# Optimization experiments

Hardware: AMD Instinct MI355X
Metric: run time of the kernel (lower is better)

## Reference

```python
import jax, jax.numpy as jnp
import numpy as np

# Detect.__init__ defaults from the source
TOP_K = 5000
CONF_THRESH = 0.01
NMS_THRESH = 0.3
VAR0, VAR1 = 0.1, 0.2   # variance = [0.1, 0.2]
NUM_CLASSES = 2

B = 16
IMAGE = 1280
FMAPS = [320, 160, 80, 40, 20, 10]          # image / steps [4,8,16,32,64,128]
MIN_SIZES = [16, 32, 64, 128, 256, 512]
AR = 1.5                                     # aspect_ratios = [[1.5]] * 6


def make_priors():
    """Vectorized PriorBox.forward: 1 prior per location (max_sizes=[], single AR)."""
    chunks = []
    for f, ms in zip(FMAPS, MIN_SIZES):
        c = (np.arange(f, dtype=np.float32) + 0.5) / f
        cy, cx = np.meshgrid(c, c, indexing='ij')
        s = ms / float(IMAGE)
        w = np.full_like(cx, s / np.sqrt(AR))   # s_k / sqrt(ar)
        h = np.full_like(cx, s * np.sqrt(AR))   # s_k * sqrt(ar)
        chunks.append(np.stack([cx, cy, w, h], -1).reshape(-1, 4))
    pr = np.concatenate(chunks, 0).clip(0.0, 1.0)   # clip=True
    return jnp.asarray(pr, jnp.float32)             # [136500, 4]


def setup_inputs() -> dict:
    key = jax.random.key(0)
    k1, k2 = jax.random.split(key)
    P = sum(f * f for f in FMAPS)   # 136500
    loc_data = 0.5 * jax.random.normal(k1, (B, P, 4), jnp.float32)
    conf_data = jax.random.uniform(k2, (B * P, NUM_CLASSES), jnp.float32)  # post-softmax probs
    prior_data = make_priors()
    return {"loc_data": loc_data, "conf_data": conf_data, "prior_data": prior_data}


def _decode(loc, priors):
    # SSD box decode with variances [0.1, 0.2]; loc, priors: [P,4]
    cxcy = priors[:, :2] + loc[:, :2] * VAR0 * priors[:, 2:]
    wh = priors[:, 2:] * jnp.exp(loc[:, 2:] * VAR1)
    xy1 = cxcy - wh * 0.5
    xy2 = xy1 + wh
    return jnp.concatenate([xy1, xy2], axis=-1)   # [P,4] x1y1x2y2


def _greedy_keep(boxes, valid):
    # Greedy NMS over score-sorted candidates. boxes [K,4], valid [K] bool.
    # Indices/keep decisions are discrete -> computed on stop_gradient'd boxes.
    b = jax.lax.stop_gradient(boxes)
    x1, y1, x2, y2 = b[:, 0], b[:, 1], b[:, 2], b[:, 3]
    area = (x2 - x1) * (y2 - y1)
    idxs = jnp.arange(b.shape[0])

    def body(keep, i):
        iw = jnp.maximum(jnp.minimum(x2, x2[i]) - jnp.maximum(x1, x1[i]), 0.0)
        ih = jnp.maximum(jnp.minimum(y2, y2[i]) - jnp.maximum(y1, y1[i]), 0.0)
        inter = iw * ih
        iou = inter / (area + area[i] - inter)
        suppress = keep[i] & (iou > NMS_THRESH) & (idxs > i)
        return keep & ~suppress, None

    keep, _ = jax.lax.scan(body, valid, idxs)
    return keep


def _detect_one(loc_i, conf_cl, priors):
    # loc_i [P,4]; conf_cl [P] = class-1 scores; returns [TOP_K, 5] (score, x1,y1,x2,y2)
    boxes = _decode(loc_i, priors)
    masked = jnp.where(conf_cl > CONF_THRESH, conf_cl, -1.0)   # c_mask gating
    order = jnp.argsort(-jax.lax.stop_gradient(masked))[:TOP_K]  # scores.sort, top_k cap
    s = masked[order]
    b = boxes[order]
    valid = s > CONF_THRESH
    keep = _greedy_keep(b, valid)
    # scatter kept (score, box) rows, in descending-score order, into dense output
    rank = jnp.cumsum(keep) - 1
    row = jnp.where(keep, rank, TOP_K)            # dropped rows -> scratch slot
    vals = jnp.concatenate([s[:, None], b], axis=1)
    vals = jnp.where(keep[:, None], vals, 0.0)
    out = jnp.zeros((TOP_K + 1, 5), jnp.float32).at[row].set(vals)
    return out[:TOP_K]


def reference(loc_data, conf_data, prior_data):
    num = loc_data.shape[0]
    P = prior_data.shape[0]
    conf_preds = conf_data.reshape(num, P, NUM_CLASSES).transpose(0, 2, 1)  # [B,2,P]
    cls1 = jax.vmap(_detect_one, in_axes=(0, 0, None))(loc_data, conf_preds[:, 1, :], prior_data)
    bg = jnp.zeros_like(cls1)                     # background class row stays zero
    output = jnp.stack([bg, cls1], axis=1)        # [B, 2, TOP_K, 5]
    # NOTE: the original's final `flt[(rank < top_k)...].fill_(0)` fills a boolean-indexed
    # COPY in torch, so it is a no-op on `output`; we faithfully return output unchanged.
    return output
```

## Files before the change

kernel.cpp:

```cpp
#include <hip/hip_runtime.h>
#include <math.h>

#pragma clang fp contract(off)

#define PNUM 136500
#define HPNUM 68250
#define BNUM 16
#define TOPK 5000
#define CAP 8192
#define NB4 4096
#define WBASE 0x2F000u
#define GCS 4
#define NWORDS 79
#define NW32 158
#define GSTRIDE 32
#define CAPE 65536
#define ELDS 10240
#define NXB 128
#define NWC 8
#define NXB2 1024
#define BSTRIDE 5120
#define EBUF 3072
#define SLOTS 4
#define SKI(i) ((i) + ((i) >> 4))

#define OFF_SC    ((size_t)0)
#define OFF_BOX4  (OFF_SC + 320000)
#define OFF_HIST  (OFF_BOX4 + 1280000)
#define OFF_GBCUR (OFF_HIST + 262144)
#define OFF_ECNT  (OFF_GBCUR + 1048576)
#define OFF_BCNT  (OFF_ECNT + 2048)
#define OFF_BCUR  (OFF_BCNT + 65536)
#define OFF_WCNT  (OFF_BCUR + 65536)
#define OFF_ZEND  (OFF_WCNT + 64)
#define OFF_CUT   (OFF_ZEND)
#define OFF_SBASE (OFF_CUT + 64)
#define OFF_WL    (OFF_SBASE + 262144)
#define OFF_KEYS  (OFF_WL + 262144)
#define OFF_EDGE  (OFF_KEYS + 1048576)
#define OFF_GRP   (OFF_EDGE + 4194304)
#define OFF_BOFS  (OFF_GRP)
#define OFF_SIDX  (OFF_GRP + 16384)
#define OFF_SBOX  (OFF_SIDX + 327680)

__device__ __forceinline__ unsigned f2ord(float f) {
    unsigned u = __float_as_uint(f);
    return (u & 0x80000000u) ? ~u : (u | 0x80000000u);
}
__device__ __forceinline__ float ord2f(unsigned o) {
    unsigned u = (o & 0x80000000u) ? (o ^ 0x80000000u) : ~o;
    return __uint_as_float(u);
}
__device__ __forceinline__ int bucketOf(float x) {
    int b = (int)((x + 0.6f) * 71.111115f);
    return (b < 0) ? 0 : ((b > 127) ? 127 : b);
}
__device__ __forceinline__ int rkeyOf(float x1, float x2) {
    int b = bucketOf(x1);
    int wc = bucketOf(x2) - b;
    if (wc > NWC - 1) wc = NWC - 1;
    if (wc < 0) wc = 0;
    return b * NWC + wc;
}

__global__ void __launch_bounds__(512) k_hist(const float* __restrict__ conf,
                                              unsigned* __restrict__ hist) {
    __shared__ unsigned lh[NB4];
    int img = blockIdx.y;
    for (int i = threadIdx.x; i < NB4; i += 512) lh[i] = 0;
    __syncthreads();
    const float4* src = (const float4*)(conf + (size_t)img * PNUM * 2);
    int stride = gridDim.x * 512;
    for (int q = blockIdx.x * 512 + threadIdx.x; q < HPNUM; q += stride) {
        float4 v = src[q];
        if (v.y > 0.01f) atomicAdd(&lh[(f2ord(v.y) >> 14) - WBASE], 1u);
        if (v.w > 0.01f) atomicAdd(&lh[(f2ord(v.w) >> 14) - WBASE], 1u);
    }
    __syncthreads();
    unsigned* h = hist + (size_t)img * NB4;
    for (int i = threadIdx.x; i < NB4; i += 512) {
        unsigned c = lh[i];
        if (c) atomicAdd(&h[i], c);
    }
}

__global__ void __launch_bounds__(256) k_cutoff2(const unsigned* __restrict__ hist,
                                                 unsigned* __restrict__ cut,
                                                 unsigned* __restrict__ sbase,
                                                 unsigned* __restrict__ wl,
                                                 unsigned* __restrict__ wcnt) {
    __shared__ unsigned csum[256], suf[256], scut;
    int img = blockIdx.x;
    int t = threadIdx.x;
    const unsigned* h = hist + (size_t)img * NB4;
    unsigned hv[16];
    unsigned s = 0;
    #pragma unroll
    for (int j = 0; j < 16; ++j) { hv[j] = h[t * 16 + j]; s += hv[j]; }
    csum[t] = s;
    __syncthreads();
    if (t == 0) {
        unsigned a = 0;
        for (int g = 255; g >= 0; --g) { unsigned c = csum[g]; suf[g] = a; a += c; }
        unsigned acc = 0, before = 0;
        int c = -1;
        for (int cc = 255; cc >= 0; --cc) {
            if (acc + csum[cc] >= (unsigned)TOPK) { c = cc; before = acc; break; }
            acc += csum[cc];
        }
        unsigned cutb = WBASE;
        if (c >= 0) {
            unsigned s2 = before;
            cutb = WBASE + (unsigned)c * 16u;
            for (int b = c * 16 + 15; b >= c * 16; --b) {
                s2 += h[b];
                if (s2 >= (unsigned)TOPK) { cutb = WBASE + (unsigned)b; break; }
            }
        }
        scut = cutb;
        cut[img] = cutb;
    }
    __syncthreads();
    unsigned cutb = scut;
    unsigned acc = suf[t];
    unsigned* sb = sbase + (size_t)img * NB4 + t * 16;
    sb[15] = acc;
    #pragma unroll
    for (int j = 14; j >= 0; --j) { acc += hv[j + 1]; sb[j] = acc; }
    #pragma unroll
    for (int j = 0; j < 16; ++j) {
        unsigned b = (unsigned)t * 16u + (unsigned)j;
        if (WBASE + b >= cutb && hv[j] > 0) {
            unsigned x = atomicAdd(wcnt, 1u);
            wl[x] = ((unsigned)img << 12) | b;
        }
    }
}

__global__ void __launch_bounds__(256) k_gather2(
        const float* __restrict__ conf, const unsigned* __restrict__ cut,
        const unsigned* __restrict__ sbase, unsigned* __restrict__ gbcur,
        unsigned long long* __restrict__ keys) {
    int q = blockIdx.x * 256 + threadIdx.x;
    int img = blockIdx.y;
    if (q >= HPNUM) return;
    unsigned cutb = cut[img];
    float4 v = ((const float4*)(conf + (size_t)img * PNUM * 2))[q];
    const unsigned* sb = sbase + (size_t)img * NB4;
    unsigned* gc = gbcur + (size_t)img * NB4 * GCS;
    unsigned long long* kp = keys + (size_t)img * CAP;
    #pragma unroll
    for (int e = 0; e < 2; ++e) {
        float s = e ? v.w : v.y;
        if (s > 0.01f) {
            unsigned o = f2ord(s);
            unsigned w18 = o >> 14;
            if (w18 >= cutb) {
                unsigned wb = w18 - WBASE;
                unsigned pos = sb[wb] + atomicAdd(&gc[wb * GCS], 1u);
                if (pos < (unsigned)CAP)
                    kp[pos] = ((unsigned long long)o << 32)
                              | (unsigned)(~(unsigned)(2 * q + e));
            }
        }
    }
}

__global__ void __launch_bounds__(256) k_ssortdec(
        const unsigned long long* __restrict__ keys,
        const unsigned* __restrict__ hist, const unsigned* __restrict__ sbase,
        const unsigned* __restrict__ wl, const unsigned* __restrict__ wcnt,
        const float* __restrict__ loc, const float* __restrict__ pri,
        float* __restrict__ SC, float4* __restrict__ BOX4,
        unsigned* __restrict__ bcnt) {
    __shared__ unsigned long long sk[1088];
    __shared__ unsigned lhist[NXB2];
    int tid = threadIdx.x;
    unsigned nW = *wcnt;
    for (unsigned w = blockIdx.x; w < nW; w += gridDim.x) {
        unsigned ent = wl[w];
        int img = (int)(ent >> 12);
        int b = (int)(ent & 4095u);
        unsigned cnt = hist[(size_t)img * NB4 + b];
        unsigned base = sbase[(size_t)img * NB4 + b];
        if (base >= (unsigned)TOPK) continue;
        const unsigned long long* kp = keys + (size_t)img * CAP + base;
        for (int i = tid; i < NXB2; i += 256) lhist[i] = 0;
        unsigned scnt = cnt > 1024 ? 1024u : cnt;
        if (scnt >= 2) {
            unsigned np2 = 2;
            while (np2 < scnt) np2 <<= 1;
            for (unsigned i = tid; i < np2; i += 256)
                sk[SKI(i)] = (i < scnt) ? kp[i] : 0ull;
            __syncthreads();
            for (unsigned k = 2; k <= np2; k <<= 1) {
                for (unsigned j = k >> 1; j > 0; j >>= 1) {
                    for (unsigned t = tid; t < (np2 >> 1); t += 256) {
                        unsigned i = ((t & ~(j - 1)) << 1) | (t & (j - 1));
                        unsigned p = i | j;
                        bool desc = ((i & k) == 0);
                        unsigned long long a = sk[SKI(i)], bb = sk[SKI(p)];
                        bool sw = desc ? (a < bb) : (a > bb);
                        if (sw) { sk[SKI(i)] = bb; sk[SKI(p)] = a; }
                    }
                    __syncthreads();
                }
            }
        } else {
            if (tid == 0 && scnt == 1) sk[0] = kp[0];
            __syncthreads();
        }
        size_t ibase = (size_t)img * TOPK;
        for (unsigned i = tid; i < cnt; i += 256) {
            unsigned r = base + i;
            if (r >= (unsigned)TOPK) continue;
            unsigned long long key = (i < scnt) ? sk[SKI(i)] : kp[i];
            float s, x1, y1, x2, y2;
            if (key != 0ull) {
                unsigned ordv = (unsigned)(key >> 32);
                s = ord2f(ordv);
                unsigned p = ~(unsigned)(key & 0xFFFFFFFFull);
                const float* lp = loc + ((size_t)img * PNUM + p) * 4;
                const float* pp = pri + (size_t)p * 4;
                float lx = lp[0], ly = lp[1], lw = lp[2], lh = lp[3];
                float px = pp[0], py = pp[1], pw = pp[2], ph = pp[3];
                float cx = px + (lx * 0.1f) * pw;
                float cy = py + (ly * 0.1f) * ph;
                float w2 = pw * expf(lw * 0.2f);
                float h2 = ph * expf(lh * 0.2f);
                x1 = cx - w2 * 0.5f;
                y1 = cy - h2 * 0.5f;
                x2 = x1 + w2;
                y2 = y1 + h2;
            } else {
                s = -1.0f; x1 = 0.f; y1 = 0.f; x2 = 0.f; y2 = 0.f;
            }
            SC[ibase + r] = s;
            BOX4[ibase + r] = make_float4(x1, y1, x2, y2);
            atomicAdd(&lhist[rkeyOf(x1, x2)], 1u);
        }
        __syncthreads();
        for (int i = tid; i < NXB2; i += 256) {
            unsigned c = lhist[i];
            if (c) atomicAdd(&bcnt[img * NXB2 + i], c);
        }
        __syncthreads();
    }
}

__global__ void __launch_bounds__(256) k_bscat(
        const unsigned* __restrict__ bcnt, unsigned* __restrict__ bcur,
        const float4* __restrict__ BOX4,
        unsigned* __restrict__ bofs, unsigned* __restrict__ sidx,
        float4* __restrict__ sbox) {
    __shared__ unsigned bpre[NXB2 + 1], tsum[256];
    int img = blockIdx.y;
    int tid = threadIdx.x;
    const unsigned* bc = bcnt + img * NXB2;
    unsigned l0 = bc[tid * 4], l1 = bc[tid * 4 + 1],
             l2 = bc[tid * 4 + 2], l3 = bc[tid * 4 + 3];
    tsum[tid] = l0 + l1 + l2 + l3;
    __syncthreads();
    if (tid == 0) {
        unsigned a = 0;
        for (int t = 0; t < 256; ++t) { unsigned c = tsum[t]; tsum[t] = a; a += c; }
        bpre[NXB2] = a;
    }
    __syncthreads();
    unsigned a = tsum[tid];
    bpre[tid * 4] = a;
    bpre[tid * 4 + 1] = a + l0;
    bpre[tid * 4 + 2] = a + l0 + l1;
    bpre[tid * 4 + 3] = a + l0 + l1 + l2;
    __syncthreads();
    if (blockIdx.x == 0) {
        if (tid < NXB) bofs[img * 130 + tid] = bpre[tid * NWC];
        if (tid == 0) bofs[img * 130 + NXB] = bpre[NXB2];
    }
    int r = blockIdx.x * 256 + tid;
    if (r < TOPK) {
        float4 b = BOX4[(size_t)img * TOPK + r];
        int bk = rkeyOf(b.x, b.z);
        unsigned s = bpre[bk] + atomicAdd(&bcur[img * NXB2 + bk], 1u);
        int base = img * BSTRIDE;
        sidx[base + s] = (unsigned)r;
        sbox[base + s] = b;
    }
}

__global__ void __launch_bounds__(256) k_pair4(
        const unsigned* __restrict__ bofs, const unsigned* __restrict__ sidx,
        const float4* __restrict__ sbox,
        unsigned* __restrict__ ecnt, unsigned* __restrict__ edges) {
    __shared__ unsigned ebuf[EBUF];
    __shared__ unsigned ecl, ebase;
    int img = blockIdx.y;
    int wid = threadIdx.x >> 6;
    int lane = threadIdx.x & 63;
    int sb0 = (blockIdx.x * 4 + wid) * SLOTS;
    if (threadIdx.x == 0) ecl = 0;
    __syncthreads();
    unsigned* ec = ecnt + (size_t)img * GSTRIDE;
    unsigned* eg = edges + (size_t)img * CAPE;
    if (sb0 < TOPK) {
        int base = img * BSTRIDE;
        float x1k[SLOTS], x2k[SLOTS], y1k[SLOTS], y2k[SLOTS], ark[SLOTS];
        unsigned rk[SLOTS];
        bool act[SLOTS];
        #pragma unroll
        for (int k = 0; k < SLOTS; ++k) {
            act[k] = (sb0 + k) < TOPK;
            int s = act[k] ? (sb0 + k) : sb0;
            float4 bk = sbox[base + s];
            x1k[k] = bk.x; y1k[k] = bk.y; x2k[k] = bk.z; y2k[k] = bk.w;
            ark[k] = (bk.z - bk.x) * (bk.w - bk.y);
            rk[k] = sidx[base + s];
        }
        int b1 = bucketOf(x1k[0]);
        int b2m = bucketOf(x2k[0]);
        #pragma unroll
        for (int k = 1; k < SLOTS; ++k)
            if (act[k]) { int b = bucketOf(x2k[k]); if (b > b2m) b2m = b; }
        const unsigned* bo = bofs + img * 130;
        unsigned s0 = bo[b1], s1 = bo[b2m + 1];
        if (s0 < s1) {
            unsigned nit = (s1 - s0 + 63) >> 6;
            unsigned c0 = s0 + (unsigned)lane;
            if (c0 > s1 - 1) c0 = s1 - 1;
            float4 cb = sbox[base + c0];
            unsigned cr = sidx[base + c0];
            for (unsigned it = 0; it < nit; ++it) {
                float4 nb = cb; unsigned nr = cr;
                if (it + 1 < nit) {
                    unsigned cn = s0 + (it + 1) * 64 + (unsigned)lane;
                    if (cn > s1 - 1) cn = s1 - 1;
                    nb = sbox[base + cn];
                    nr = sidx[base + cn];
                }
                bool in = (s0 + it * 64 + (unsigned)lane) < s1;
                float bar = (cb.z - cb.x) * (cb.w - cb.y);
                #pragma unroll
                for (int k = 0; k < SLOTS; ++k) {
                    bool hit = false;
                    unsigned edge = 0;
                    if (in && act[k] && cb.x >= x1k[k]
                        && !(cb.x == x1k[k] && cr <= rk[k])) {
                        float dx = fminf(x2k[k], cb.z) - fmaxf(x1k[k], cb.x);
                        if (dx > 0.0f) {
                            float dy = fminf(y2k[k], cb.w) - fmaxf(y1k[k], cb.y);
                            if (dy > 0.0f) {
                                float inter = dx * dy;
                                float iou = inter / (bar + ark[k] - inter);
                                if (iou > 0.3f) {
                                    unsigned su = (rk[k] < cr) ? rk[k] : cr;
                                    unsigned vi = (rk[k] < cr) ? cr : rk[k];
                                    edge = (vi << 13) | su;
                                    hit = true;
                                }
                            }
                        }
                    }
                    unsigned long long bal = __ballot(hit);
                    if (bal) {
                        int n = __popcll(bal);
                        unsigned wb = 0;
                        if (lane == 0) wb = atomicAdd(&ecl, (unsigned)n);
                        wb = __shfl(wb, 0, 64);
                        if (hit) {
                            unsigned long long lt =
                                (lane == 0) ? 0ull : ((1ull << lane) - 1ull);
                            unsigned p = wb + (unsigned)__popcll(bal & lt);
                            if (p < (unsigned)EBUF) ebuf[p] = edge;
                            else {
                                unsigned gp = atomicAdd(ec, 1u);
                                if (gp < (unsigned)CAPE) eg[gp] = edge;
                            }
                        }
                    }
                }
                cb = nb; cr = nr;
            }
        }
    }
    __syncthreads();
    unsigned n = min(ecl, (unsigned)EBUF);
    if (threadIdx.x == 0 && n) ebase = atomicAdd(ec, n);
    __syncthreads();
    for (unsigned i = threadIdx.x; i < n; i += 256) {
        unsigned p = ebase + i;
        if (p < (unsigned)CAPE) eg[p] = ebuf[i];
    }
}

__global__ void __launch_bounds__(256) k_nms3(
        const float* __restrict__ SC, const float4* __restrict__ BOX4,
        const unsigned* __restrict__ ecnt, const unsigned* __restrict__ edges,
        float* __restrict__ out) {
    __shared__ unsigned lgrp[ELDS];
    __shared__ unsigned undL[160], keptL[160], blockL[160];
    __shared__ unsigned pfx[80];
    __shared__ int chg[2];
    int img = blockIdx.x;
    int tid = threadIdx.x;
    int l = tid & 63;
    int wid = tid >> 6;
    size_t ib = (size_t)img * TOPK;
    const float* sc = SC + ib;

    float* oimg = out + (size_t)img * 2 * TOPK * 5;
    uint4* oz = (uint4*)oimg;
    uint4 z4 = make_uint4(0u, 0u, 0u, 0u);
    for (int i = tid; i < 12500; i += 256) oz[i] = z4;

    if (tid < 160) { keptL[tid] = 0u; blockL[tid] = 0u; }
    if (tid < 2) chg[tid] = 0;
    for (int w = wid; w < NWORDS; w += 4) {
        int row = w * 64 + l;
        bool valid = (row < TOPK) && (sc[row] > 0.01f);
        unsigned long long b = __ballot(valid);
        if (l == 0) {
            undL[2 * w]     = (unsigned)b;
            undL[2 * w + 1] = (unsigned)(b >> 32);
        }
    }
    unsigned E = min(ecnt[(size_t)img * GSTRIDE], (unsigned)CAPE);
    const unsigned* eimg = edges + (size_t)img * CAPE;
    bool inl = (E <= (unsigned)ELDS);
    if (inl) for (unsigned e = tid; e < E; e += 256) lgrp[e] = eimg[e];
    __syncthreads();

    for (int round = 0; round < 256; ++round) {
        int par = round & 1;
        for (unsigned e = tid; e < E; e += 256) {
            unsigned ed = inl ? lgrp[e] : eimg[e];
            unsigned s = ed & 8191u;
            unsigned v = ed >> 13;
            unsigned sw = s >> 5, sb = s & 31u;
            unsigned vw = v >> 5, vb = 1u << (v & 31u);
            if ((keptL[sw] >> sb) & 1u) {
                if (undL[vw] & vb) {
                    unsigned old = atomicAnd(&undL[vw], ~vb);
                    if (old & vb) chg[par] = 1;
                }
            } else if ((undL[sw] >> sb) & 1u) {
                if (!(blockL[vw] & vb)) atomicOr(&blockL[vw], vb);
            }
        }
        __syncthreads();
        if (tid < NW32) {
            unsigned nk = undL[tid] & ~blockL[tid];
            if (nk) {
                keptL[tid] |= nk;
                undL[tid] &= ~nk;
                chg[par] = 1;
            }
            blockL[tid] = 0u;
        }
        if (tid == 0) chg[par ^ 1] = 0;
        __syncthreads();
        if (!chg[par]) break;
    }

    if (tid == 0) {
        unsigned acc = 0;
        for (int w = 0; w < NWORDS; ++w) {
            pfx[w] = acc;
            acc += (unsigned)(__popc(keptL[2 * w]) + __popc(keptL[2 * w + 1]));
        }
    }
    __syncthreads();
    const float4* bx = BOX4 + ib;
    float* op = oimg + (size_t)TOPK * 5;
    for (int w = wid; w < NWORDS; w += 4) {
        unsigned long long kw =
            ((unsigned long long)keptL[2 * w + 1] << 32) | keptL[2 * w];
        if (!kw) continue;
        int row = w * 64 + l;
        if ((kw >> l) & 1ull) {
            int rank = (int)pfx[w] + (int)__popcll(kw & ((1ull << l) - 1ull));
            float4 b = bx[row];
            float* r = op + (size_t)rank * 5;
            r[0] = sc[row]; r[1] = b.x; r[2] = b.y; r[3] = b.z; r[4] = b.w;
        }
    }
}

extern "C" void kernel_launch(void* const* d_in, const int* in_sizes, int n_in,
                              void* d_out, int out_size, void* d_ws, size_t ws_size,
                              hipStream_t stream) {
    (void)in_sizes; (void)n_in; (void)ws_size; (void)out_size;
    const float* loc  = (const float*)d_in[0];
    const float* conf = (const float*)d_in[1];
    const float* pri  = (const float*)d_in[2];
    float* out = (float*)d_out;
    char* ws = (char*)d_ws;

    float* SC   = (float*)(ws + OFF_SC);
    float4* BOX4 = (float4*)(ws + OFF_BOX4);
    unsigned* hist = (unsigned*)(ws + OFF_HIST);
    unsigned* cut  = (unsigned*)(ws + OFF_CUT);
    unsigned* sbase = (unsigned*)(ws + OFF_SBASE);
    unsigned* gbcur = (unsigned*)(ws + OFF_GBCUR);
    unsigned long long* keys = (unsigned long long*)(ws + OFF_KEYS);
    unsigned* ecnt = (unsigned*)(ws + OFF_ECNT);
    unsigned* bcnt = (unsigned*)(ws + OFF_BCNT);
    unsigned* bcur = (unsigned*)(ws + OFF_BCUR);
    unsigned* wcnt = (unsigned*)(ws + OFF_WCNT);
    unsigned* wl   = (unsigned*)(ws + OFF_WL);
    unsigned* edges = (unsigned*)(ws + OFF_EDGE);
    unsigned* bofs = (unsigned*)(ws + OFF_BOFS);
    unsigned* sidx = (unsigned*)(ws + OFF_SIDX);
    float4* sbox = (float4*)(ws + OFF_SBOX);

    hipMemsetAsync(ws + OFF_HIST, 0, OFF_ZEND - OFF_HIST, stream);

    dim3 gh1(16, BNUM);
    k_hist<<<gh1, 512, 0, stream>>>(conf, hist);
    k_cutoff2<<<BNUM, 256, 0, stream>>>(hist, cut, sbase, wl, wcnt);
    dim3 gh2((HPNUM + 255) / 256, BNUM);
    k_gather2<<<gh2, 256, 0, stream>>>(conf, cut, sbase, gbcur, keys);
    k_ssortdec<<<1024, 256, 0, stream>>>(keys, hist, sbase, wl, wcnt,
                                         loc, pri, SC, BOX4, bcnt);
    dim3 gb((TOPK + 255) / 256, BNUM);
    k_bscat<<<gb, 256, 0, stream>>>(bcnt, bcur, BOX4, bofs, sidx, sbox);
    dim3 pg((TOPK + 4 * SLOTS - 1) / (4 * SLOTS), BNUM);
    k_pair4<<<pg, 256, 0, stream>>>(bofs, sidx, sbox, ecnt, edges);
    k_nms3<<<BNUM, 256, 0, stream>>>(SC, BOX4, ecnt, edges, out);
}
```

Before: 212.6 us.

## Add y-range sub-buckets, y-overlap reject, and move output zeroing to bscat

The bucket key gains a third dimension, an 8-way y1 range, so boxes are sorted by x bucket, then width class, then y range. The pair kernel computes the y extent of its slot group and skips candidates that cannot overlap vertically before doing the IoU work. Output zeroing moves from the 16-block NMS kernel to the wider k_bscat grid, so it no longer sits on the serial NMS path. Smaller changes: the histogram grid is doubled and the LDS edge cap is raised. In exchange, the per-block bucket histogram grows from 1024 to 8192 entries, which makes the flush in k_ssortdec, the prefix scan in k_bscat and the workspace memset larger.

```diff
diff --git a/kernel.cpp b/kernel.cpp
--- a/kernel.cpp
+++ b/kernel.cpp
@@ -15,10 +15,11 @@
 #define NW32 158
 #define GSTRIDE 32
 #define CAPE 65536
-#define ELDS 10240
+#define ELDS 14336
 #define NXB 128
 #define NWC 8
-#define NXB2 1024
+#define NYR 8
+#define NXB2 8192
 #define BSTRIDE 5120
 #define EBUF 3072
 #define SLOTS 4
@@ -30,8 +31,8 @@
 #define OFF_GBCUR (OFF_HIST + 262144)
 #define OFF_ECNT  (OFF_GBCUR + 1048576)
 #define OFF_BCNT  (OFF_ECNT + 2048)
-#define OFF_BCUR  (OFF_BCNT + 65536)
-#define OFF_WCNT  (OFF_BCUR + 65536)
+#define OFF_BCUR  (OFF_BCNT + 524288)
+#define OFF_WCNT  (OFF_BCUR + 524288)
 #define OFF_ZEND  (OFF_WCNT + 64)
 #define OFF_CUT   (OFF_ZEND)
 #define OFF_SBASE (OFF_CUT + 64)
@@ -55,12 +56,15 @@
     int b = (int)((x + 0.6f) * 71.111115f);
     return (b < 0) ? 0 : ((b > 127) ? 127 : b);
 }
-__device__ __forceinline__ int rkeyOf(float x1, float x2) {
+__device__ __forceinline__ int rkeyOf(float x1, float x2, float y1) {
     int b = bucketOf(x1);
     int wc = bucketOf(x2) - b;
     if (wc > NWC - 1) wc = NWC - 1;
     if (wc < 0) wc = 0;
-    return b * NWC + wc;
+    int yr = (int)((y1 + 0.6f) * 4.4444447f);
+    if (yr < 0) yr = 0;
+    if (yr > NYR - 1) yr = NYR - 1;
+    return (b * NWC + wc) * NYR + yr;
 }
 
 __global__ void __launch_bounds__(512) k_hist(const float* __restrict__ conf,
@@ -237,7 +241,7 @@
             }
             SC[ibase + r] = s;
             BOX4[ibase + r] = make_float4(x1, y1, x2, y2);
-            atomicAdd(&lhist[rkeyOf(x1, x2)], 1u);
+            atomicAdd(&lhist[rkeyOf(x1, x2, y1)], 1u);
         }
         __syncthreads();
         for (int i = tid; i < NXB2; i += 256) {
@@ -252,14 +256,19 @@
         const unsigned* __restrict__ bcnt, unsigned* __restrict__ bcur,
         const float4* __restrict__ BOX4,
         unsigned* __restrict__ bofs, unsigned* __restrict__ sidx,
-        float4* __restrict__ sbox) {
+        float4* __restrict__ sbox, float* __restrict__ out) {
     __shared__ unsigned bpre[NXB2 + 1], tsum[256];
     int img = blockIdx.y;
     int tid = threadIdx.x;
-    const unsigned* bc = bcnt + img * NXB2;
-    unsigned l0 = bc[tid * 4], l1 = bc[tid * 4 + 1],
-             l2 = bc[tid * 4 + 2], l3 = bc[tid * 4 + 3];
-    tsum[tid] = l0 + l1 + l2 + l3;
+    uint4* oz = (uint4*)(out + (size_t)img * 2 * TOPK * 5);
+    uint4 z4 = make_uint4(0u, 0u, 0u, 0u);
+    for (int i = blockIdx.x * 256 + tid; i < 12500; i += 20 * 256) oz[i] = z4;
+    const unsigned* bc = bcnt + (size_t)img * NXB2;
+    unsigned lv[32];
+    unsigned s = 0;
+    #pragma unroll
+    for (int j = 0; j < 32; ++j) { lv[j] = bc[tid * 32 + j]; s += lv[j]; }
+    tsum[tid] = s;
     __syncthreads();
     if (tid == 0) {
         unsigned a = 0;
@@ -268,23 +277,21 @@
     }
     __syncthreads();
     unsigned a = tsum[tid];
-    bpre[tid * 4] = a;
-    bpre[tid * 4 + 1] = a + l0;
-    bpre[tid * 4 + 2] = a + l0 + l1;
-    bpre[tid * 4 + 3] = a + l0 + l1 + l2;
+    #pragma unroll
+    for (int j = 0; j < 32; ++j) { bpre[tid * 32 + j] = a; a += lv[j]; }
     __syncthreads();
     if (blockIdx.x == 0) {
-        if (tid < NXB) bofs[img * 130 + tid] = bpre[tid * NWC];
+        if (tid < NXB) bofs[img * 130 + tid] = bpre[tid * (NWC * NYR)];
         if (tid == 0) bofs[img * 130 + NXB] = bpre[NXB2];
     }
     int r = blockIdx.x * 256 + tid;
     if (r < TOPK) {
         float4 b = BOX4[(size_t)img * TOPK + r];
-        int bk = rkeyOf(b.x, b.z);
-        unsigned s = bpre[bk] + atomicAdd(&bcur[img * NXB2 + bk], 1u);
+        int bk = rkeyOf(b.x, b.z, b.y);
+        unsigned sp = bpre[bk] + atomicAdd(&bcur[(size_t)img * NXB2 + bk], 1u);
         int base = img * BSTRIDE;
-        sidx[base + s] = (unsigned)r;
-        sbox[base + s] = b;
+        sidx[base + sp] = (unsigned)r;
+        sbox[base + sp] = b;
     }
 }
 
@@ -318,9 +325,14 @@
         }
         int b1 = bucketOf(x1k[0]);
         int b2m = bucketOf(x2k[0]);
+        float gymin = y1k[0], gymax = y2k[0];
         #pragma unroll
         for (int k = 1; k < SLOTS; ++k)
-            if (act[k]) { int b = bucketOf(x2k[k]); if (b > b2m) b2m = b; }
+            if (act[k]) {
+                int b = bucketOf(x2k[k]); if (b > b2m) b2m = b;
+                gymin = fminf(gymin, y1k[k]);
+                gymax = fmaxf(gymax, y2k[k]);
+            }
         const unsigned* bo = bofs + img * 130;
         unsigned s0 = bo[b1], s1 = bo[b2m + 1];
         if (s0 < s1) {
@@ -338,12 +350,13 @@
                     nr = sidx[base + cn];
                 }
                 bool in = (s0 + it * 64 + (unsigned)lane) < s1;
+                bool yok = in && (cb.w > gymin) && (cb.y < gymax);
                 float bar = (cb.z - cb.x) * (cb.w - cb.y);
                 #pragma unroll
                 for (int k = 0; k < SLOTS; ++k) {
                     bool hit = false;
                     unsigned edge = 0;
-                    if (in && act[k] && cb.x >= x1k[k]
+                    if (yok && act[k] && cb.x >= x1k[k]
                         && !(cb.x == x1k[k] && cr <= rk[k])) {
                         float dx = fminf(x2k[k], cb.z) - fmaxf(x1k[k], cb.x);
                         if (dx > 0.0f) {
@@ -407,11 +420,6 @@
     size_t ib = (size_t)img * TOPK;
     const float* sc = SC + ib;
 
-    float* oimg = out + (size_t)img * 2 * TOPK * 5;
-    uint4* oz = (uint4*)oimg;
-    uint4 z4 = make_uint4(0u, 0u, 0u, 0u);
-    for (int i = tid; i < 12500; i += 256) oz[i] = z4;
-
     if (tid < 160) { keptL[tid] = 0u; blockL[tid] = 0u; }
     if (tid < 2) chg[tid] = 0;
     for (int w = wid; w < NWORDS; w += 4) {
@@ -470,7 +478,7 @@
     }
     __syncthreads();
     const float4* bx = BOX4 + ib;
-    float* op = oimg + (size_t)TOPK * 5;
+    float* op = out + (((size_t)img * 2) + 1) * TOPK * 5;
     for (int w = wid; w < NWORDS; w += 4) {
         unsigned long long kw =
             ((unsigned long long)keptL[2 * w + 1] << 32) | keptL[2 * w];
@@ -514,7 +522,7 @@
 
     hipMemsetAsync(ws + OFF_HIST, 0, OFF_ZEND - OFF_HIST, stream);
 
-    dim3 gh1(16, BNUM);
+    dim3 gh1(32, BNUM);
     k_hist<<<gh1, 512, 0, stream>>>(conf, hist);
     k_cutoff2<<<BNUM, 256, 0, stream>>>(hist, cut, sbase, wl, wcnt);
     dim3 gh2((HPNUM + 255) / 256, BNUM);
@@ -522,7 +530,7 @@
     k_ssortdec<<<1024, 256, 0, stream>>>(keys, hist, sbase, wl, wcnt,
                                          loc, pri, SC, BOX4, bcnt);
     dim3 gb((TOPK + 255) / 256, BNUM);
-    k_bscat<<<gb, 256, 0, stream>>>(bcnt, bcur, BOX4, bofs, sidx, sbox);
+    k_bscat<<<gb, 256, 0, stream>>>(bcnt, bcur, BOX4, bofs, sidx, sbox, out);
     dim3 pg((TOPK + 4 * SLOTS - 1) / (4 * SLOTS), BNUM);
     k_pair4<<<pg, 256, 0, stream>>>(bofs, sidx, sbox, ecnt, edges);
     k_nms3<<<BNUM, 256, 0, stream>>>(SC, BOX4, ecnt, edges, out);
```

Measured after the change: 216.8 us. About the same (+2.0%).
